# Performance work log

Measured on AMD Instinct MI355X. Metric: run time of the kernel, lower is better.

The kernel has to match this reference:

```python
import math
import jax, jax.numpy as jnp
import numpy as np

NUM_HEADS = 32
NUM_KV_HEADS = 8
HEAD_SIZE = 128
FEATURE_DIM = 64
SEQ_LEN = 2048
WINDOW_SIZE = 64
EPS = 1e-12
MASK_VALUE = -100000000.0


def _make_masks(n: int, w: int):
    # block-diagonal ones(w,w) tiles, plus the rolled (sub-diagonal) tiles
    m = math.ceil(n / w)
    mask = np.kron(np.eye(m), np.ones((w, w)))
    mask = mask + np.roll(mask, -w, axis=-1)
    mask = mask[:n, :n]
    mask_window = np.tril(mask).astype(bool)[None, None]          # [1,1,n,n]
    mask_linear = np.tril(1.0 - mask).astype(bool)[None, None]    # [1,1,n,n]
    return jnp.asarray(mask_window), jnp.asarray(mask_linear)


def _feature_map(w, x):
    # f(x) = clamp(cat(softmax(xW), softmax(-xW)), min=eps)
    z = jnp.einsum('hdf,bhld->bhlf', w, x)
    return jnp.clip(
        jnp.concatenate([jax.nn.softmax(z, axis=-1), jax.nn.softmax(-z, axis=-1)], axis=-1),
        EPS, None)


def setup_inputs() -> dict:
    key = jax.random.key(0)
    ks = jax.random.split(key, 6)
    return {
        'query': jax.random.normal(ks[0], (SEQ_LEN, NUM_HEADS * HEAD_SIZE), dtype=jnp.float32),
        'key': jax.random.normal(ks[1], (SEQ_LEN, NUM_KV_HEADS * HEAD_SIZE), dtype=jnp.float32),
        'value': jax.random.normal(ks[2], (SEQ_LEN, NUM_KV_HEADS * HEAD_SIZE), dtype=jnp.float32),
        'fmap_q_w': 0.02 * jax.random.normal(ks[3], (NUM_HEADS, HEAD_SIZE, FEATURE_DIM), dtype=jnp.float32),
        'fmap_k_w': 0.02 * jax.random.normal(ks[4], (NUM_HEADS, HEAD_SIZE, FEATURE_DIM), dtype=jnp.float32),
        'window_factors': jax.random.normal(ks[5], (1, NUM_HEADS, 1, 1), dtype=jnp.float32),
    }


def reference(query, key, value, fmap_q_w, fmap_k_w, window_factors):
    T = query.shape[0]
    q = query.reshape(T, NUM_HEADS, HEAD_SIZE)
    k = key.reshape(T, NUM_KV_HEADS, HEAD_SIZE)
    v = value.reshape(T, NUM_KV_HEADS, HEAD_SIZE)
    rep = NUM_HEADS // NUM_KV_HEADS
    k = jnp.repeat(k, rep, axis=1)
    v = jnp.repeat(v, rep, axis=1)
    # [T,H,D] -> [1,H,T,D]
    q = jnp.moveaxis(q, 0, -2)[None]
    k = jnp.moveaxis(k, 0, -2)[None]
    v = jnp.moveaxis(v, 0, -2)[None]

    f_q = _feature_map(fmap_q_w, q)  # [1,H,T,2F]
    f_k = _feature_map(fmap_k_w, k)
    wf = jax.nn.sigmoid(window_factors)

    mask_window, mask_linear = _make_masks(SEQ_LEN, WINDOW_SIZE)
    mask_window = mask_window[:, :, :T, :T]
    mask_linear = mask_linear[:, :, :T, :T]

    # sliding-window softmax term
    a_sm = jnp.einsum('bhmd,bhnd->bhmn', q, k) * (HEAD_SIZE ** -0.5)
    a_sm = jnp.where(mask_window, a_sm, MASK_VALUE)
    a_sm_max = jnp.max(a_sm, axis=-1, keepdims=True)
    a_sm = wf * jnp.exp(a_sm - a_sm_max)
    sum_sm = jnp.sum(a_sm, axis=-1, keepdims=True)

    # linear feature-map term (linear_factor = 1)
    a_ln = jnp.einsum('bhmd,bhnd->bhmn', f_q, f_k)
    a_ln = jnp.where(mask_linear, a_ln, 0.0)
    sum_ln = jnp.sum(a_ln, axis=-1, keepdims=True)

    y = jnp.einsum('bhmn,bhnd->bhmd', a_sm + a_ln, v)
    return y / (sum_sm + sum_ln)
```

## Files before the change

### kernel.cpp

```cpp
#include <hip/hip_runtime.h>
#include <math.h>

#define T_SEQ 2048
#define NH    32
#define NKV   8
#define HS    128
#define FD    64
#define NBLK  32
#define EPSF  1e-12f
#define LDP   136

typedef unsigned short u16;
typedef __bf16 bf16x8 __attribute__((ext_vector_type(8)));
typedef float  f32x4  __attribute__((ext_vector_type(4)));

__device__ __forceinline__ u16 f2b(float f) {
  unsigned u = __builtin_bit_cast(unsigned, f);
  return (u16)((u + 0x7fffu + ((u >> 16) & 1u)) >> 16);
}

#define FQB_OFF 0
#define FKT_OFF 16777216
#define ST_OFF  33554432
#define VT_OFF  71303168
#define WT_OFF  75497472
#define QB_OFF  76546048
#define KB_OFF  93323264

__device__ __forceinline__ void stage_bf(u16* buf, const u16* __restrict__ src, int tid) {
#pragma unroll
  for (int i = 0; i < 4; ++i) {
    int idx = tid * 8 + i * 2048, rr = idx >> 7, c = idx & 127;
    *(uint4*)(buf + rr * LDP + c) = *(const uint4*)(src + idx);
  }
}
__device__ __forceinline__ void stage_vt(u16* buf, const u16* __restrict__ vts,
                                         int rofs, int kb0, int B, int tid) {
#pragma unroll
  for (int i = 0; i < 4; ++i) {
    int idx = tid * 8 + i * 2048, rr = idx >> 7, c = idx & 127;
    int key = (c < 64) ? (kb0 * 64 + c) : (B * 64 + (c - 64));
    *(uint4*)(buf + rr * LDP + c) = *(const uint4*)(vts + (size_t)(rr + rofs) * T_SEQ + key);
  }
}

__global__ __launch_bounds__(256) void k_pre(
    const float* __restrict__ wq, const float* __restrict__ wk,
    const float* __restrict__ vg,
    u16* __restrict__ WT, u16* __restrict__ VT)
{
  __shared__ float sB[128 * 68];
  const int bx = blockIdx.x, tid = threadIdx.x;

  if (bx < 64) {
    const int h = bx >> 1, isk = bx & 1;
    const float* src = (isk ? wk : wq) + (size_t)h * HS * FD;
    for (int idx = tid * 4; idx < 8192; idx += 1024) {
      int r = idx >> 6, c = idx & 63;
      *(float4*)(sB + r * 68 + c) = *(const float4*)(src + idx);
    }
    __syncthreads();
    u16* dst = WT + ((size_t)(isk * NH + h)) * 8192;
    for (int i = 0; i < 8; ++i) {
      int ch = tid + i * 256;
      int f = ch >> 5, d4 = (ch & 31) * 4;
      ushort4 u;
      u.x = f2b(sB[(d4 + 0) * 68 + f]);
      u.y = f2b(sB[(d4 + 1) * 68 + f]);
      u.z = f2b(sB[(d4 + 2) * 68 + f]);
      u.w = f2b(sB[(d4 + 3) * 68 + f]);
      *(ushort4*)(dst + f * 128 + d4) = u;
    }
  } else {
    const int idx2 = bx - 64;
    const int b = idx2 & 31, kvh = idx2 >> 5;
    float* sV = sB;
    for (int idx = tid * 4; idx < 8192; idx += 1024) {
      int r = idx >> 7, c = idx & 127;
      *(float4*)(sV + r * 129 + c) = *(const float4*)(vg + (size_t)(b * 64 + r) * (NKV * HS) + kvh * HS + c);
    }
    __syncthreads();
    const int lane = tid & 63, w = tid >> 6;
#pragma unroll
    for (int i = 0; i < 32; ++i) {
      int d = w * 32 + i;
      VT[((size_t)(kvh * 128 + d)) * T_SEQ + b * 64 + lane] = f2b(sV[lane * 129 + d]);
    }
  }
}

__global__ __launch_bounds__(256) void k_fmap(
    const float* __restrict__ qg, const float* __restrict__ kg,
    const u16* __restrict__ WT,
    u16* __restrict__ fqb, u16* __restrict__ FKT,
    u16* __restrict__ QB, u16* __restrict__ KBB)
{
  __shared__ __align__(16) u16 smem[2 * 64 * 136];
  u16* sX = smem;
  u16* sW = smem + 64 * 136;
  const int lt = blockIdx.x, h = blockIdx.y, isk = blockIdx.z;
  const int tid = threadIdx.x, lane = tid & 63, w = tid >> 6;
  const int quad = lane >> 4, txn = lane & 15;

  const float* xbase = isk ? (kg + (h >> 2) * HS) : (qg + h * HS);
  const int    xstr  = isk ? (NKV * HS) : (NH * HS);
  for (int idx = tid * 4; idx < 8192; idx += 1024) {
    int r = idx >> 7, c = idx & 127;
    float4 v4 = *(const float4*)(xbase + (size_t)(lt * 64 + r) * xstr + c);
    ushort4 u; u.x = f2b(v4.x); u.y = f2b(v4.y); u.z = f2b(v4.z); u.w = f2b(v4.w);
    *(ushort4*)(sX + r * 136 + c) = u;
  }
  const u16* wt = WT + ((size_t)(isk * NH + h)) * 8192;
  for (int i = 0; i < 4; ++i) {
    int ch = tid + i * 256;
    int row = ch >> 4, d8 = (ch & 15) * 8;
    *(uint4*)(sW + row * 136 + d8) = *(const uint4*)(wt + row * 128 + d8);
  }
  __syncthreads();

  if (!isk) {
    u16* ob = QB + ((size_t)(h * NBLK + lt)) * 8192;
    for (int i = 0; i < 4; ++i) {
      int ch = tid + i * 256;
      int row = ch >> 4, d8 = (ch & 15) * 8;
      *(uint4*)(ob + row * 128 + d8) = *(const uint4*)(sX + row * 136 + d8);
    }
  } else if ((h & 3) == 0) {
    u16* ob = KBB + ((size_t)((h >> 2) * NBLK + lt)) * 8192;
    for (int i = 0; i < 4; ++i) {
      int ch = tid + i * 256;
      int row = ch >> 4, d8 = (ch & 15) * 8;
      *(uint4*)(ob + row * 128 + d8) = *(const uint4*)(sX + row * 136 + d8);
    }
  }

  const int arow = w * 16 + txn;
  const f32x4 vzero = {0.f, 0.f, 0.f, 0.f};
  f32x4 zt[4] = {vzero, vzero, vzero, vzero};
#pragma unroll
  for (int ks = 0; ks < 4; ++ks) {
    bf16x8 a = *(const bf16x8*)(sX + arow * 136 + ks * 32 + quad * 8);
#pragma unroll
    for (int nt = 0; nt < 4; ++nt) {
      bf16x8 bb = *(const bf16x8*)(sW + (nt * 16 + txn) * 136 + ks * 32 + quad * 8);
      zt[nt] = __builtin_amdgcn_mfma_f32_16x16x32_bf16(a, bb, zt[nt], 0, 0, 0);
    }
  }

  float E1[4][4], E2[4][4];
#pragma unroll
  for (int r = 0; r < 4; ++r) {
    float zv[4];
    float mx = -1e30f, mn = 1e30f;
#pragma unroll
    for (int nt = 0; nt < 4; ++nt) {
      zv[nt] = zt[nt][r];
      mx = fmaxf(mx, zv[nt]); mn = fminf(mn, zv[nt]);
    }
#pragma unroll
    for (int o = 1; o < 16; o <<= 1) {
      mx = fmaxf(mx, __shfl_xor(mx, o));
      mn = fminf(mn, __shfl_xor(mn, o));
    }
    float e1[4], e2[4], s1 = 0.f, s2 = 0.f;
#pragma unroll
    for (int nt = 0; nt < 4; ++nt) {
      e1[nt] = __expf(zv[nt] - mx); s1 += e1[nt];
      e2[nt] = __expf(mn - zv[nt]); s2 += e2[nt];
    }
#pragma unroll
    for (int o = 1; o < 16; o <<= 1) { s1 += __shfl_xor(s1, o); s2 += __shfl_xor(s2, o); }
    float r1 = 1.f / s1, r2 = 1.f / s2;
#pragma unroll
    for (int nt = 0; nt < 4; ++nt) {
      E1[r][nt] = fmaxf(e1[nt] * r1, EPSF);
      E2[r][nt] = fmaxf(e2[nt] * r2, EPSF);
    }
  }

  __syncthreads();

  if (!isk) {
#pragma unroll
    for (int r = 0; r < 4; ++r) {
      int row = w * 16 + quad * 4 + r;
#pragma unroll
      for (int nt = 0; nt < 4; ++nt) {
        sX[row * 136 + nt * 16 + txn]      = f2b(E1[r][nt]);
        sX[row * 136 + 64 + nt * 16 + txn] = f2b(E2[r][nt]);
      }
    }
    __syncthreads();
    u16* ob = fqb + ((size_t)(h * NBLK + lt)) * 8192;
    for (int i = 0; i < 4; ++i) {
      int ch = tid + i * 256;
      int row = ch >> 4, f8 = (ch & 15) * 8;
      *(uint4*)(ob + row * 128 + f8) = *(const uint4*)(sX + row * 136 + f8);
    }
  } else {
#pragma unroll
    for (int r = 0; r < 4; ++r) {
      int j = w * 16 + quad * 4 + r;
#pragma unroll
      for (int nt = 0; nt < 4; ++nt) {
        sX[(nt * 16 + txn) * 68 + j]        = f2b(E1[r][nt]);
        sX[(nt * 16 + txn + 64) * 68 + j]   = f2b(E2[r][nt]);
      }
    }
    __syncthreads();
    u16* ob = FKT + (size_t)h * 128 * T_SEQ + lt * 64;
    for (int i = 0; i < 8; ++i) {
      int ch = tid + i * 256;
      int row = ch >> 4, j4 = (ch & 15) * 4;
      *(ushort4*)(ob + (size_t)row * T_SEQ + j4) = *(const ushort4*)(sX + row * 68 + j4);
    }
  }
}

__global__ __launch_bounds__(256) void k_scan(
    const u16* __restrict__ FKT, const u16* __restrict__ VT, u16* __restrict__ ST)
{
  __shared__ __align__(16) u16 sVT[16 * 72];
  __shared__ __align__(16) u16 sFK[64 * 72];
  const int dc = blockIdx.x, fh = blockIdx.y, h = blockIdx.z;
  const int tid = threadIdx.x, lane = tid & 63, w = tid >> 6;
  const int quad = lane >> 4, txn = lane & 15;
  const bool doz = (dc == 0);

  bf16x8 vone;
#pragma unroll
  for (int j = 0; j < 8; ++j) vone[j] = (__bf16)1.0f;

  const u16* vbase = VT + ((size_t)((h >> 2) * 128 + dc * 16)) * T_SEQ;
  const u16* fbase = FKT + ((size_t)(h * 128 + fh * 64)) * T_SEQ;

  const int srow = tid >> 4, sj4 = (tid & 15) * 4;
  ushort4 rv, rf[4];
  rv = *(const ushort4*)(vbase + (size_t)srow * T_SEQ + sj4);
#pragma unroll
  for (int i = 0; i < 4; ++i) {
    int ch = tid + i * 256;
    int fr = ch >> 4, fj4 = (ch & 15) * 4;
    rf[i] = *(const ushort4*)(fbase + (size_t)fr * T_SEQ + fj4);
  }

  const f32x4 vzero = {0.f, 0.f, 0.f, 0.f};
  f32x4 acc = vzero, zacc = vzero;

  for (int b = 0; b < NBLK; ++b) {
    __syncthreads();
    *(ushort4*)(sVT + srow * 72 + sj4) = rv;
#pragma unroll
    for (int i = 0; i < 4; ++i) {
      int ch = tid + i * 256;
      int fr = ch >> 4, fj4 = (ch & 15) * 4;
      *(ushort4*)(sFK + fr * 72 + fj4) = rf[i];
    }
    __syncthreads();
    if (b + 1 < NBLK) {
      rv = *(const ushort4*)(vbase + (size_t)srow * T_SEQ + (b + 1) * 64 + sj4);
#pragma unroll
      for (int i = 0; i < 4; ++i) {
        int ch = tid + i * 256;
        int fr = ch >> 4, fj4 = (ch & 15) * 4;
        rf[i] = *(const ushort4*)(fbase + (size_t)fr * T_SEQ + (b + 1) * 64 + fj4);
      }
    }
#pragma unroll
    for (int ks = 0; ks < 2; ++ks) {
      bf16x8 a  = *(const bf16x8*)(sVT + txn * 72 + ks * 32 + quad * 8);
      bf16x8 bb = *(const bf16x8*)(sFK + (w * 16 + txn) * 72 + ks * 32 + quad * 8);
      acc = __builtin_amdgcn_mfma_f32_16x16x32_bf16(a, bb, acc, 0, 0, 0);
      if (doz) zacc = __builtin_amdgcn_mfma_f32_16x16x32_bf16(vone, bb, zacc, 0, 0, 0);
    }
    u16* Sb = ST + (((size_t)(h * NBLK + b)) * 144 + dc * 16) * 128 + fh * 64;
#pragma unroll
    for (int r = 0; r < 4; ++r)
      Sb[(quad * 4 + r) * 128 + w * 16 + txn] = f2b(acc[r]);
    if (doz && quad == 0)
      ST[(((size_t)(h * NBLK + b)) * 144 + 128) * 128 + fh * 64 + w * 16 + txn] = f2b(zacc[0]);
  }
}

__global__ __launch_bounds__(256, 4) void k_main(
    const u16* __restrict__ QB, const u16* __restrict__ KBB,
    const u16* __restrict__ fqb, const u16* __restrict__ ST, const u16* __restrict__ VT,
    const float* __restrict__ wfac, float* __restrict__ out)
{
  __shared__ __align__(16) u16 RA[64 * LDP];
  __shared__ __align__(16) u16 RB[64 * LDP];
  __shared__ __align__(16) u16 sz[128];
  const int B = blockIdx.x, h = blockIdx.y, tid = threadIdx.x;
  const int lane = tid & 63, w = tid >> 6;
  const int quad = lane >> 4, txn = lane & 15;
  const int arow = w * 16 + txn;
  const int koff = quad * 8;

  const f32x4 vzero = {0.f, 0.f, 0.f, 0.f};
  f32x4 y[8];
#pragma unroll
  for (int t = 0; t < 8; ++t) y[t] = vzero;
  float sln[4] = {0.f, 0.f, 0.f, 0.f};
  const bf16x8 bzero = {0, 0, 0, 0, 0, 0, 0, 0};

  const int kb0 = (B >= 1) ? B - 1 : 0;
  const u16* qtile = QB  + ((size_t)(h * NBLK + B)) * 8192;
  const u16* ktB   = KBB + ((size_t)((h >> 2) * NBLK + B)) * 8192;
  const u16* ktP   = KBB + ((size_t)((h >> 2) * NBLK + kb0)) * 8192;
  const u16* vts   = VT  + (size_t)((h >> 2) * 128) * T_SEQ;

  if (B >= 2) {
    const u16* fsrc = fqb + ((size_t)(h * NBLK + B)) * 8192;
    const u16* ssrc = ST + ((size_t)(h * NBLK + (B - 2))) * 18432;
    stage_bf(RA, fsrc, tid);
    stage_bf(RB, ssrc, tid);
    if (tid < 32) *(ushort4*)(sz + tid * 4) = *(const ushort4*)(ssrc + 16384 + tid * 4);
    __syncthreads();
    f32x4 yz = vzero;
#pragma unroll
    for (int ks = 0; ks < 4; ++ks) {
      bf16x8 a = *(const bf16x8*)(RA + arow * LDP + ks * 32 + koff);
#pragma unroll
      for (int t = 0; t < 4; ++t) {
        bf16x8 bb = *(const bf16x8*)(RB + (t * 16 + txn) * LDP + ks * 32 + koff);
        y[t] = __builtin_amdgcn_mfma_f32_16x16x32_bf16(a, bb, y[t], 0, 0, 0);
      }
      bf16x8 bz = (txn == 0) ? *(const bf16x8*)(sz + ks * 32 + koff) : bzero;
      yz = __builtin_amdgcn_mfma_f32_16x16x32_bf16(a, bz, yz, 0, 0, 0);
    }
    __syncthreads();
    stage_bf(RB, ssrc + 8192, tid);
    __syncthreads();
#pragma unroll
    for (int ks = 0; ks < 4; ++ks) {
      bf16x8 a = *(const bf16x8*)(RA + arow * LDP + ks * 32 + koff);
#pragma unroll
      for (int t = 4; t < 8; ++t) {
        bf16x8 bb = *(const bf16x8*)(RB + (t * 16 + txn - 64) * LDP + ks * 32 + koff);
        y[t] = __builtin_amdgcn_mfma_f32_16x16x32_bf16(a, bb, y[t], 0, 0, 0);
      }
    }
#pragma unroll
    for (int r = 0; r < 4; ++r) sln[r] = __shfl(yz[r], lane & 48);
    __syncthreads();
  }

  stage_bf(RA, qtile, tid);
  stage_bf(RB, ktB, tid);
  __syncthreads();

  f32x4 s[8];
#pragma unroll
  for (int t = 0; t < 8; ++t) s[t] = vzero;
#pragma unroll
  for (int ks = 0; ks < 4; ++ks) {
    bf16x8 a = *(const bf16x8*)(RA + arow * LDP + ks * 32 + koff);
#pragma unroll
    for (int t = 0; t < 4; ++t) {
      bf16x8 bb = *(const bf16x8*)(RB + (t * 16 + txn) * LDP + ks * 32 + koff);
      s[4 + t] = __builtin_amdgcn_mfma_f32_16x16x32_bf16(a, bb, s[4 + t], 0, 0, 0);
    }
  }

  if (B >= 1) {
    __syncthreads();
    stage_bf(RB, ktP, tid);
    __syncthreads();
#pragma unroll
    for (int ks = 0; ks < 4; ++ks) {
      bf16x8 a = *(const bf16x8*)(RA + arow * LDP + ks * 32 + koff);
#pragma unroll
      for (int t = 0; t < 4; ++t) {
        bf16x8 bb = *(const bf16x8*)(RB + (t * 16 + txn) * LDP + ks * 32 + koff);
        s[t] = __builtin_amdgcn_mfma_f32_16x16x32_bf16(a, bb, s[t], 0, 0, 0);
      }
    }
  }

  float wf = wfac[h];
  wf = 1.f / (1.f + __expf(-wf));
  const float scale = 0.08838834764831845f;
  float ssum[4];
#pragma unroll
  for (int r = 0; r < 4; ++r) {
    const int irow = w * 16 + quad * 4 + r;
    float sv[8];
    float m = -1e30f;
#pragma unroll
    for (int t = 0; t < 8; ++t) {
      float x = s[t][r] * scale;
      bool msk = (t < 4) ? (B == 0) : ((t - 4) * 16 + txn > irow);
      x = msk ? -1e30f : x;
      sv[t] = x;
      m = fmaxf(m, x);
    }
#pragma unroll
    for (int o = 1; o < 16; o <<= 1) m = fmaxf(m, __shfl_xor(m, o));
    float ss = 0.f;
#pragma unroll
    for (int t = 0; t < 8; ++t) {
      float e = (sv[t] > -1e29f) ? wf * __expf(sv[t] - m) : 0.f;
      ss += e;
      RA[irow * LDP + t * 16 + txn] = f2b(e);
    }
#pragma unroll
    for (int o = 1; o < 16; o <<= 1) ss += __shfl_xor(ss, o);
    ssum[r] = ss;
  }
  __syncthreads();

  stage_vt(RB, vts, 0, kb0, B, tid);
  __syncthreads();
#pragma unroll
  for (int ks = 0; ks < 4; ++ks) {
    if (B == 0 && ks < 2) continue;
    bf16x8 a = *(const bf16x8*)(RA + arow * LDP + ks * 32 + koff);
#pragma unroll
    for (int t = 0; t < 4; ++t) {
      bf16x8 bb = *(const bf16x8*)(RB + (t * 16 + txn) * LDP + ks * 32 + koff);
      y[t] = __builtin_amdgcn_mfma_f32_16x16x32_bf16(a, bb, y[t], 0, 0, 0);
    }
  }
  __syncthreads();

  stage_vt(RB, vts, 64, kb0, B, tid);
  __syncthreads();
#pragma unroll
  for (int ks = 0; ks < 4; ++ks) {
    if (B == 0 && ks < 2) continue;
    bf16x8 a = *(const bf16x8*)(RA + arow * LDP + ks * 32 + koff);
#pragma unroll
    for (int t = 4; t < 8; ++t) {
      bf16x8 bb = *(const bf16x8*)(RB + (t * 16 + txn - 64) * LDP + ks * 32 + koff);
      y[t] = __builtin_amdgcn_mfma_f32_16x16x32_bf16(a, bb, y[t], 0, 0, 0);
    }
  }

  const size_t obase = ((size_t)h * T_SEQ + B * 64) * HS;
#pragma unroll
  for (int r = 0; r < 4; ++r) {
    float inv = 1.f / (ssum[r] + sln[r]);
    int irow = w * 16 + quad * 4 + r;
#pragma unroll
    for (int t = 0; t < 8; ++t)
      out[obase + (size_t)irow * HS + t * 16 + txn] = y[t][r] * inv;
  }
}

extern "C" void kernel_launch(void* const* d_in, const int* in_sizes, int n_in,
                              void* d_out, int out_size, void* d_ws, size_t ws_size,
                              hipStream_t stream) {
  const float* q    = (const float*)d_in[0];
  const float* k    = (const float*)d_in[1];
  const float* v    = (const float*)d_in[2];
  const float* wq   = (const float*)d_in[3];
  const float* wk   = (const float*)d_in[4];
  const float* wfac = (const float*)d_in[5];
  float* out = (float*)d_out;
  char* wsb = (char*)d_ws;

  u16* fqb = (u16*)(wsb + FQB_OFF);
  u16* FKT = (u16*)(wsb + FKT_OFF);
  u16* ST  = (u16*)(wsb + ST_OFF);
  u16* VT  = (u16*)(wsb + VT_OFF);
  u16* WT  = (u16*)(wsb + WT_OFF);
  u16* QB  = (u16*)(wsb + QB_OFF);
  u16* KBB = (u16*)(wsb + KB_OFF);

  k_pre  <<<dim3(320),         256, 0, stream>>>(wq, wk, v, WT, VT);
  k_fmap <<<dim3(NBLK, NH, 2), 256, 0, stream>>>(q, k, WT, fqb, FKT, QB, KBB);
  k_scan <<<dim3(8, 2, NH),    256, 0, stream>>>(FKT, VT, ST);
  k_main <<<dim3(NBLK, NH),    256, 0, stream>>>(QB, KBB, fqb, ST, VT, wfac, out);
}
```

Before: 167.4 us.

## Fuse query feature map and bf16 conversion into main attention kernel

```diff
diff --git a/kernel.cpp b/kernel.cpp
--- a/kernel.cpp
+++ b/kernel.cpp
@@ -7,6 +7,7 @@
 #define HS    128
 #define FD    64
 #define NBLK  32
+#define SCAN_NB 30
 #define EPSF  1e-12f
 #define LDP   136
 
@@ -19,13 +20,11 @@
   return (u16)((u + 0x7fffu + ((u >> 16) & 1u)) >> 16);
 }
 
-#define FQB_OFF 0
-#define FKT_OFF 16777216
-#define ST_OFF  33554432
-#define VT_OFF  71303168
-#define WT_OFF  75497472
-#define QB_OFF  76546048
-#define KB_OFF  93323264
+#define FKT_OFF 0
+#define ST_OFF  16777216
+#define VT_OFF  54525952
+#define WT_OFF  58720256
+#define KB_OFF  59768832
 
 __device__ __forceinline__ void stage_bf(u16* buf, const u16* __restrict__ src, int tid) {
 #pragma unroll
@@ -90,27 +89,25 @@
 }
 
 __global__ __launch_bounds__(256) void k_fmap(
-    const float* __restrict__ qg, const float* __restrict__ kg,
-    const u16* __restrict__ WT,
-    u16* __restrict__ fqb, u16* __restrict__ FKT,
-    u16* __restrict__ QB, u16* __restrict__ KBB)
+    const float* __restrict__ kg, const u16* __restrict__ WT,
+    u16* __restrict__ FKT, u16* __restrict__ KBB)
 {
   __shared__ __align__(16) u16 smem[2 * 64 * 136];
   u16* sX = smem;
   u16* sW = smem + 64 * 136;
-  const int lt = blockIdx.x, h = blockIdx.y, isk = blockIdx.z;
+  const int lt = blockIdx.x, h = blockIdx.y;
   const int tid = threadIdx.x, lane = tid & 63, w = tid >> 6;
   const int quad = lane >> 4, txn = lane & 15;
 
-  const float* xbase = isk ? (kg + (h >> 2) * HS) : (qg + h * HS);
-  const int    xstr  = isk ? (NKV * HS) : (NH * HS);
+  const float* xbase = kg + (h >> 2) * HS;
+  const int    xstr  = NKV * HS;
   for (int idx = tid * 4; idx < 8192; idx += 1024) {
     int r = idx >> 7, c = idx & 127;
     float4 v4 = *(const float4*)(xbase + (size_t)(lt * 64 + r) * xstr + c);
     ushort4 u; u.x = f2b(v4.x); u.y = f2b(v4.y); u.z = f2b(v4.z); u.w = f2b(v4.w);
     *(ushort4*)(sX + r * 136 + c) = u;
   }
-  const u16* wt = WT + ((size_t)(isk * NH + h)) * 8192;
+  const u16* wt = WT + ((size_t)(NH + h)) * 8192;
   for (int i = 0; i < 4; ++i) {
     int ch = tid + i * 256;
     int row = ch >> 4, d8 = (ch & 15) * 8;
@@ -118,14 +115,7 @@
   }
   __syncthreads();
 
-  if (!isk) {
-    u16* ob = QB + ((size_t)(h * NBLK + lt)) * 8192;
-    for (int i = 0; i < 4; ++i) {
-      int ch = tid + i * 256;
-      int row = ch >> 4, d8 = (ch & 15) * 8;
-      *(uint4*)(ob + row * 128 + d8) = *(const uint4*)(sX + row * 136 + d8);
-    }
-  } else if ((h & 3) == 0) {
+  if ((h & 3) == 0) {
     u16* ob = KBB + ((size_t)((h >> 2) * NBLK + lt)) * 8192;
     for (int i = 0; i < 4; ++i) {
       int ch = tid + i * 256;
@@ -180,40 +170,21 @@
 
   __syncthreads();
 
-  if (!isk) {
-#pragma unroll
-    for (int r = 0; r < 4; ++r) {
-      int row = w * 16 + quad * 4 + r;
-#pragma unroll
-      for (int nt = 0; nt < 4; ++nt) {
-        sX[row * 136 + nt * 16 + txn]      = f2b(E1[r][nt]);
-        sX[row * 136 + 64 + nt * 16 + txn] = f2b(E2[r][nt]);
-      }
-    }
-    __syncthreads();
-    u16* ob = fqb + ((size_t)(h * NBLK + lt)) * 8192;
-    for (int i = 0; i < 4; ++i) {
-      int ch = tid + i * 256;
-      int row = ch >> 4, f8 = (ch & 15) * 8;
-      *(uint4*)(ob + row * 128 + f8) = *(const uint4*)(sX + row * 136 + f8);
-    }
-  } else {
-#pragma unroll
-    for (int r = 0; r < 4; ++r) {
-      int j = w * 16 + quad * 4 + r;
-#pragma unroll
-      for (int nt = 0; nt < 4; ++nt) {
-        sX[(nt * 16 + txn) * 68 + j]        = f2b(E1[r][nt]);
-        sX[(nt * 16 + txn + 64) * 68 + j]   = f2b(E2[r][nt]);
-      }
-    }
-    __syncthreads();
-    u16* ob = FKT + (size_t)h * 128 * T_SEQ + lt * 64;
-    for (int i = 0; i < 8; ++i) {
-      int ch = tid + i * 256;
-      int row = ch >> 4, j4 = (ch & 15) * 4;
-      *(ushort4*)(ob + (size_t)row * T_SEQ + j4) = *(const ushort4*)(sX + row * 68 + j4);
-    }
+#pragma unroll
+  for (int r = 0; r < 4; ++r) {
+    int j = w * 16 + quad * 4 + r;
+#pragma unroll
+    for (int nt = 0; nt < 4; ++nt) {
+      sX[(nt * 16 + txn) * 68 + j]        = f2b(E1[r][nt]);
+      sX[(nt * 16 + txn + 64) * 68 + j]   = f2b(E2[r][nt]);
+    }
+  }
+  __syncthreads();
+  u16* ob = FKT + (size_t)h * 128 * T_SEQ + lt * 64;
+  for (int i = 0; i < 8; ++i) {
+    int ch = tid + i * 256;
+    int row = ch >> 4, j4 = (ch & 15) * 4;
+    *(ushort4*)(ob + (size_t)row * T_SEQ + j4) = *(const ushort4*)(sX + row * 68 + j4);
   }
 }
 
@@ -247,7 +218,7 @@
   const f32x4 vzero = {0.f, 0.f, 0.f, 0.f};
   f32x4 acc = vzero, zacc = vzero;
 
-  for (int b = 0; b < NBLK; ++b) {
+  for (int b = 0; b < SCAN_NB; ++b) {
     __syncthreads();
     *(ushort4*)(sVT + srow * 72 + sj4) = rv;
 #pragma unroll
@@ -257,7 +228,7 @@
       *(ushort4*)(sFK + fr * 72 + fj4) = rf[i];
     }
     __syncthreads();
-    if (b + 1 < NBLK) {
+    if (b + 1 < SCAN_NB) {
       rv = *(const ushort4*)(vbase + (size_t)srow * T_SEQ + (b + 1) * 64 + sj4);
 #pragma unroll
       for (int i = 0; i < 4; ++i) {
@@ -283,9 +254,10 @@
 }
 
 __global__ __launch_bounds__(256, 4) void k_main(
-    const u16* __restrict__ QB, const u16* __restrict__ KBB,
-    const u16* __restrict__ fqb, const u16* __restrict__ ST, const u16* __restrict__ VT,
-    const float* __restrict__ wfac, float* __restrict__ out)
+    const float* __restrict__ qg, const u16* __restrict__ KBB,
+    const u16* __restrict__ WT, const u16* __restrict__ ST,
+    const u16* __restrict__ VT, const float* __restrict__ wfac,
+    float* __restrict__ out)
 {
   __shared__ __align__(16) u16 RA[64 * LDP];
   __shared__ __align__(16) u16 RB[64 * LDP];
@@ -304,49 +276,67 @@
   const bf16x8 bzero = {0, 0, 0, 0, 0, 0, 0, 0};
 
   const int kb0 = (B >= 1) ? B - 1 : 0;
-  const u16* qtile = QB  + ((size_t)(h * NBLK + B)) * 8192;
   const u16* ktB   = KBB + ((size_t)((h >> 2) * NBLK + B)) * 8192;
   const u16* ktP   = KBB + ((size_t)((h >> 2) * NBLK + kb0)) * 8192;
   const u16* vts   = VT  + (size_t)((h >> 2) * 128) * T_SEQ;
 
+  for (int idx = tid * 4; idx < 8192; idx += 1024) {
+    int r = idx >> 7, c = idx & 127;
+    float4 v4 = *(const float4*)(qg + (size_t)(B * 64 + r) * (NH * HS) + h * HS + c);
+    ushort4 u; u.x = f2b(v4.x); u.y = f2b(v4.y); u.z = f2b(v4.z); u.w = f2b(v4.w);
+    *(ushort4*)(RA + r * LDP + c) = u;
+  }
+  if (B >= 2) stage_bf(RB, WT + (size_t)h * 8192, tid);
+  __syncthreads();
+
+  f32x4 zt[4] = {vzero, vzero, vzero, vzero};
   if (B >= 2) {
-    const u16* fsrc = fqb + ((size_t)(h * NBLK + B)) * 8192;
-    const u16* ssrc = ST + ((size_t)(h * NBLK + (B - 2))) * 18432;
-    stage_bf(RA, fsrc, tid);
-    stage_bf(RB, ssrc, tid);
-    if (tid < 32) *(ushort4*)(sz + tid * 4) = *(const ushort4*)(ssrc + 16384 + tid * 4);
-    __syncthreads();
-    f32x4 yz = vzero;
 #pragma unroll
     for (int ks = 0; ks < 4; ++ks) {
       bf16x8 a = *(const bf16x8*)(RA + arow * LDP + ks * 32 + koff);
 #pragma unroll
-      for (int t = 0; t < 4; ++t) {
-        bf16x8 bb = *(const bf16x8*)(RB + (t * 16 + txn) * LDP + ks * 32 + koff);
-        y[t] = __builtin_amdgcn_mfma_f32_16x16x32_bf16(a, bb, y[t], 0, 0, 0);
-      }
-      bf16x8 bz = (txn == 0) ? *(const bf16x8*)(sz + ks * 32 + koff) : bzero;
-      yz = __builtin_amdgcn_mfma_f32_16x16x32_bf16(a, bz, yz, 0, 0, 0);
-    }
-    __syncthreads();
-    stage_bf(RB, ssrc + 8192, tid);
-    __syncthreads();
-#pragma unroll
-    for (int ks = 0; ks < 4; ++ks) {
-      bf16x8 a = *(const bf16x8*)(RA + arow * LDP + ks * 32 + koff);
-#pragma unroll
-      for (int t = 4; t < 8; ++t) {
-        bf16x8 bb = *(const bf16x8*)(RB + (t * 16 + txn - 64) * LDP + ks * 32 + koff);
-        y[t] = __builtin_amdgcn_mfma_f32_16x16x32_bf16(a, bb, y[t], 0, 0, 0);
-      }
-    }
-#pragma unroll
-    for (int r = 0; r < 4; ++r) sln[r] = __shfl(yz[r], lane & 48);
-    __syncthreads();
-  }
-
-  stage_bf(RA, qtile, tid);
+      for (int nt = 0; nt < 4; ++nt) {
+        bf16x8 bb = *(const bf16x8*)(RB + (nt * 16 + txn) * LDP + ks * 32 + koff);
+        zt[nt] = __builtin_amdgcn_mfma_f32_16x16x32_bf16(a, bb, zt[nt], 0, 0, 0);
+      }
+    }
+  }
+  __syncthreads();
   stage_bf(RB, ktB, tid);
+
+  unsigned Epk[4][4];
+  if (B >= 2) {
+#pragma unroll
+    for (int r = 0; r < 4; ++r) {
+      float zv[4];
+      float mx = -1e30f, mn = 1e30f;
+#pragma unroll
+      for (int nt = 0; nt < 4; ++nt) {
+        zv[nt] = zt[nt][r];
+        mx = fmaxf(mx, zv[nt]); mn = fminf(mn, zv[nt]);
+      }
+#pragma unroll
+      for (int o = 1; o < 16; o <<= 1) {
+        mx = fmaxf(mx, __shfl_xor(mx, o));
+        mn = fminf(mn, __shfl_xor(mn, o));
+      }
+      float e1[4], e2[4], s1 = 0.f, s2 = 0.f;
+#pragma unroll
+      for (int nt = 0; nt < 4; ++nt) {
+        e1[nt] = __expf(zv[nt] - mx); s1 += e1[nt];
+        e2[nt] = __expf(mn - zv[nt]); s2 += e2[nt];
+      }
+#pragma unroll
+      for (int o = 1; o < 16; o <<= 1) { s1 += __shfl_xor(s1, o); s2 += __shfl_xor(s2, o); }
+      float r1 = 1.f / s1, r2 = 1.f / s2;
+#pragma unroll
+      for (int nt = 0; nt < 4; ++nt) {
+        unsigned lo = f2b(fmaxf(e1[nt] * r1, EPSF));
+        unsigned hi = f2b(fmaxf(e2[nt] * r2, EPSF));
+        Epk[r][nt] = lo | (hi << 16);
+      }
+    }
+  }
   __syncthreads();
 
   f32x4 s[8];
@@ -434,6 +424,49 @@
       bf16x8 bb = *(const bf16x8*)(RB + (t * 16 + txn - 64) * LDP + ks * 32 + koff);
       y[t] = __builtin_amdgcn_mfma_f32_16x16x32_bf16(a, bb, y[t], 0, 0, 0);
     }
+  }
+
+  if (B >= 2) {
+    __syncthreads();
+#pragma unroll
+    for (int r = 0; r < 4; ++r) {
+      int row = w * 16 + quad * 4 + r;
+#pragma unroll
+      for (int nt = 0; nt < 4; ++nt) {
+        RA[row * LDP + nt * 16 + txn]      = (u16)(Epk[r][nt] & 0xffffu);
+        RA[row * LDP + 64 + nt * 16 + txn] = (u16)(Epk[r][nt] >> 16);
+      }
+    }
+    const u16* ssrc = ST + ((size_t)(h * NBLK + (B - 2))) * 18432;
+    stage_bf(RB, ssrc, tid);
+    if (tid < 32) *(ushort4*)(sz + tid * 4) = *(const ushort4*)(ssrc + 16384 + tid * 4);
+    __syncthreads();
+    f32x4 yz = vzero;
+#pragma unroll
+    for (int ks = 0; ks < 4; ++ks) {
+      bf16x8 a = *(const bf16x8*)(RA + arow * LDP + ks * 32 + koff);
+#pragma unroll
+      for (int t = 0; t < 4; ++t) {
+        bf16x8 bb = *(const bf16x8*)(RB + (t * 16 + txn) * LDP + ks * 32 + koff);
+        y[t] = __builtin_amdgcn_mfma_f32_16x16x32_bf16(a, bb, y[t], 0, 0, 0);
+      }
+      bf16x8 bz = (txn == 0) ? *(const bf16x8*)(sz + ks * 32 + koff) : bzero;
+      yz = __builtin_amdgcn_mfma_f32_16x16x32_bf16(a, bz, yz, 0, 0, 0);
+    }
+    __syncthreads();
+    stage_bf(RB, ssrc + 8192, tid);
+    __syncthreads();
+#pragma unroll
+    for (int ks = 0; ks < 4; ++ks) {
+      bf16x8 a = *(const bf16x8*)(RA + arow * LDP + ks * 32 + koff);
+#pragma unroll
+      for (int t = 4; t < 8; ++t) {
+        bf16x8 bb = *(const bf16x8*)(RB + (t * 16 + txn - 64) * LDP + ks * 32 + koff);
+        y[t] = __builtin_amdgcn_mfma_f32_16x16x32_bf16(a, bb, y[t], 0, 0, 0);
+      }
+    }
+#pragma unroll
+    for (int r = 0; r < 4; ++r) sln[r] = __shfl(yz[r], lane & 48);
   }
 
   const size_t obase = ((size_t)h * T_SEQ + B * 64) * HS;
@@ -459,16 +492,14 @@
   float* out = (float*)d_out;
   char* wsb = (char*)d_ws;
 
-  u16* fqb = (u16*)(wsb + FQB_OFF);
   u16* FKT = (u16*)(wsb + FKT_OFF);
   u16* ST  = (u16*)(wsb + ST_OFF);
   u16* VT  = (u16*)(wsb + VT_OFF);
   u16* WT  = (u16*)(wsb + WT_OFF);
-  u16* QB  = (u16*)(wsb + QB_OFF);
   u16* KBB = (u16*)(wsb + KB_OFF);
 
-  k_pre  <<<dim3(320),         256, 0, stream>>>(wq, wk, v, WT, VT);
-  k_fmap <<<dim3(NBLK, NH, 2), 256, 0, stream>>>(q, k, WT, fqb, FKT, QB, KBB);
-  k_scan <<<dim3(8, 2, NH),    256, 0, stream>>>(FKT, VT, ST);
-  k_main <<<dim3(NBLK, NH),    256, 0, stream>>>(QB, KBB, fqb, ST, VT, wfac, out);
-}
+  k_pre  <<<dim3(320),      256, 0, stream>>>(wq, wk, v, WT, VT);
+  k_fmap <<<dim3(NBLK, NH), 256, 0, stream>>>(k, WT, FKT, KBB);
+  k_scan <<<dim3(8, 2, NH), 256, 0, stream>>>(FKT, VT, ST);
+  k_main <<<dim3(NBLK, NH), 256, 0, stream>>>(q, KBB, WT, ST, VT, wfac, out);
+}
```

New measurement: 164.2 us. About the same (-1.9%).
